# Optimization experiments

Measured on AMD Instinct MI355X. Metric: run time of the kernel, lower is better.

Reference implementation:

```python
import jax, jax.numpy as jnp
import numpy as np

N_NODES = 50000
N_EDGES = 800000
D = 128
N_LAYERS = 3
BN_EPS = 1e-5


def setup_inputs() -> dict:
    key = jax.random.key(0)
    ks = jax.random.split(key, 12)
    x = jax.random.normal(ks[0], (N_NODES, D), dtype=jnp.float32)
    edge_index = jax.random.randint(ks[1], (2, N_EDGES), 0, N_NODES, dtype=jnp.int64)
    edge_attr = jnp.zeros((N_EDGES,), dtype=jnp.int32)  # unused by BaseGIN
    edge_weight = jax.random.uniform(ks[2], (N_EDGES,), dtype=jnp.float32)
    s = 1.0 / np.sqrt(D)
    W1 = jax.random.uniform(ks[3], (N_LAYERS, D, D), minval=-s, maxval=s, dtype=jnp.float32)
    b1 = jax.random.uniform(ks[4], (N_LAYERS, D), minval=-s, maxval=s, dtype=jnp.float32)
    W2 = jax.random.uniform(ks[5], (N_LAYERS, D, D), minval=-s, maxval=s, dtype=jnp.float32)
    b2 = jax.random.uniform(ks[6], (N_LAYERS, D), minval=-s, maxval=s, dtype=jnp.float32)
    eps = jnp.zeros((N_LAYERS,), dtype=jnp.float32)          # GIN epsilon, init 0
    gamma = jnp.ones((N_LAYERS, D), dtype=jnp.float32)       # BN weight
    beta = jnp.zeros((N_LAYERS, D), dtype=jnp.float32)       # BN bias
    return {"x": x, "edge_index": edge_index, "edge_attr": edge_attr,
            "edge_weight": edge_weight, "W1": W1, "b1": b1, "W2": W2,
            "b2": b2, "eps": eps, "gamma": gamma, "beta": beta}


def reference(x, edge_index, edge_attr, edge_weight, W1, b1, W2, b2, eps, gamma, beta):
    del edge_attr  # deleted in BaseGIN.forward
    src, dst = edge_index[0], edge_index[1]
    ew = edge_weight[:, None]  # [E, 1], matches edge_weight[:, None] in torch
    n = x.shape[0]
    for i in range(N_LAYERS):
        # GINConv: propagate = scatter-add of gathered x[src] * edge_weight
        msg = x[src] * ew                                   # [E, D]
        agg = jax.ops.segment_sum(msg, dst, num_segments=n)  # [N, D]
        h = (1.0 + eps[i]) * x + agg
        # MLP: Linear -> ReLU -> Linear
        h = jnp.maximum(h @ W1[i] + b1[i], 0.0) @ W2[i] + b2[i]
        # BatchNorm1d (training-mode batch statistics, biased variance)
        mu = jnp.mean(h, axis=0)
        var = jnp.mean((h - mu) ** 2, axis=0)
        h = gamma[i] * (h - mu) * jax.lax.rsqrt(var + BN_EPS) + beta[i]
        h = jnp.maximum(h, 0.0)  # ReLU (dropout p=0.0 -> identity)
        x = x + h  # residual
    return x
```

## Files before the change

kernel.cpp:

```cpp
#include <hip/hip_runtime.h>

#define NN 50000
#define NE 800000
#define DD 128
#define D4 32
#define NBUCK 196
#define CAP 5120
#define BIN_EDGES 2048

typedef __attribute__((ext_vector_type(8))) short short8;
typedef __attribute__((ext_vector_type(4))) float f32x4;

__device__ __forceinline__ unsigned short f2bf(float f) {
    unsigned u = __float_as_uint(f);
    unsigned r = u + 0x7FFF + ((u >> 16) & 1);
    return (unsigned short)(r >> 16);
}
__device__ __forceinline__ float bf2f(unsigned short s) {
    return __uint_as_float(((unsigned)s) << 16);
}


__global__ void x2b(const float4* __restrict__ xin, ushort4* __restrict__ xb) {
    int i = blockIdx.x * blockDim.x + threadIdx.x;
    if (i >= NN * D4) return;
    float4 v = xin[i];
    ushort4 o;
    o.x = f2bf(v.x); o.y = f2bf(v.y); o.z = f2bf(v.z); o.w = f2bf(v.w);
    xb[i] = o;
}


__global__ void prep_wt(const float* __restrict__ W1, const float* __restrict__ W2,
                        unsigned short* __restrict__ Wt) {
    int i = blockIdx.x * blockDim.x + threadIdx.x;
    if (i >= 6 * 16384) return;
    int m = i >> 14;
    int r = i & 16383;
    int n = r >> 7;
    int k = r & 127;
    const float* Ws = (m < 3) ? (W1 + m * 16384) : (W2 + (m - 3) * 16384);
    Wt[i] = f2bf(Ws[k * 128 + n]);
}


__global__ void init_bcur(int* __restrict__ bcur) {
    int t = threadIdx.x;
    if (t < NBUCK) bcur[t] = t * CAP;
}

__global__ void __launch_bounds__(256) bin_pass(const int* __restrict__ ei,
                                                const float* __restrict__ ew,
                                                int* __restrict__ bcur,
                                                int2* __restrict__ staging) {
    __shared__ int cnt[256], base[256], cur[256];
    int tid = threadIdx.x;
    int e0 = blockIdx.x * BIN_EDGES;
    int ne = NE - e0; if (ne > BIN_EDGES) ne = BIN_EDGES;
    cnt[tid] = 0;
    cur[tid] = 0;
    __syncthreads();
    int dstv[BIN_EDGES / 256];
    unsigned packv[BIN_EDGES / 256];
#pragma unroll
    for (int j = 0; j < BIN_EDGES / 256; j++) {
        int i = j * 256 + tid;
        dstv[j] = -1;
        if (i < ne) {
            int e = e0 + i;
            int dst = ei[NE + e];
            dstv[j] = dst;
            packv[j] = (((unsigned)ei[e]) << 16) | (unsigned)f2bf(ew[e]);
            atomicAdd(&cnt[dst >> 8], 1);
        }
    }
    __syncthreads();
    if (tid < NBUCK && cnt[tid] > 0) base[tid] = atomicAdd(&bcur[tid], cnt[tid]);
    __syncthreads();
#pragma unroll
    for (int j = 0; j < BIN_EDGES / 256; j++) {
        int dst = dstv[j];
        if (dst >= 0) {
            int b = dst >> 8;
            int p = atomicAdd(&cur[b], 1);
            staging[base[b] + p] = make_int2((int)packv[j], dst & 255);
        }
    }
}

__global__ void scan_buckets(const int* __restrict__ bcur, int* __restrict__ bb2) {
    __shared__ int sh[256];
    int tid = threadIdx.x;
    int c = (tid < NBUCK) ? (bcur[tid] - tid * CAP) : 0;
    sh[tid] = c;
    __syncthreads();
    for (int o = 1; o < 256; o <<= 1) {
        int v = sh[tid];
        int add = (tid >= o) ? sh[tid - o] : 0;
        __syncthreads();
        sh[tid] = v + add;
        __syncthreads();
    }
    if (tid < NBUCK) bb2[tid] = sh[tid] - c;
}

__global__ void __launch_bounds__(256) place_pass(const int2* __restrict__ staging,
                                                  const int* __restrict__ bcur,
                                                  const int* __restrict__ bb2,
                                                  int* __restrict__ rowptr,
                                                  unsigned* __restrict__ srcw) {
    __shared__ int hist[256], off[256], cur[256];
    __shared__ unsigned outb[CAP];
    int b = blockIdx.x;
    int tid = threadIdx.x;
    int sbase = b * CAP;
    int nb = bcur[b] - sbase;
    int bucketBase = bb2[b];
    hist[tid] = 0;
    __syncthreads();
    for (int i = tid; i < nb; i += 256) atomicAdd(&hist[staging[sbase + i].y], 1);
    __syncthreads();
    off[tid] = hist[tid];
    __syncthreads();
    for (int o = 1; o < 256; o <<= 1) {
        int v = off[tid];
        int add = (tid >= o) ? off[tid - o] : 0;
        __syncthreads();
        off[tid] = v + add;
        __syncthreads();
    }
    int excl = off[tid] - hist[tid];
    cur[tid] = excl;
    int node = b * 256 + tid;
    if (node < NN) rowptr[node] = bucketBase + excl;
    if (b == 0 && tid == 0) rowptr[NN] = NE;
    __syncthreads();
    for (int i = tid; i < nb; i += 256) {
        int2 r = staging[sbase + i];
        int p = atomicAdd(&cur[r.y], 1);
        outb[p] = (unsigned)r.x;
    }
    __syncthreads();
    for (int i = tid; i < nb; i += 256) srcw[bucketBase + i] = outb[i];
}


__global__ void __launch_bounds__(256) gather_kernel(
    const unsigned short* __restrict__ xb, const unsigned* __restrict__ srcw,
    const int* __restrict__ rowptr, const float* __restrict__ epsp,
    unsigned short* __restrict__ g, float* __restrict__ stats) {
    if (blockIdx.x == 0) stats[threadIdx.x] = 0.f;
    int node = blockIdx.x * 8 + (threadIdx.x >> 5);
    int lane = threadIdx.x & 31;
    if (node >= NN) return;
    float epsv = 1.0f + *epsp;
    int beg = rowptr[node], end = rowptr[node + 1];
    const ushort4* xb4 = (const ushort4*)xb;
    ushort4 xv = xb4[node * D4 + lane];
    float4 acc = make_float4(bf2f(xv.x) * epsv, bf2f(xv.y) * epsv,
                             bf2f(xv.z) * epsv, bf2f(xv.w) * epsv);
    int i = beg;
    for (; i + 1 < end; i += 2) {
        unsigned sw0 = srcw[i];
        unsigned sw1 = srcw[i + 1];
        ushort4 r0 = xb4[(sw0 >> 16) * D4 + lane];
        ushort4 r1 = xb4[(sw1 >> 16) * D4 + lane];
        float w0 = bf2f((unsigned short)(sw0 & 0xffff));
        float w1 = bf2f((unsigned short)(sw1 & 0xffff));
        acc.x += bf2f(r0.x) * w0; acc.y += bf2f(r0.y) * w0;
        acc.z += bf2f(r0.z) * w0; acc.w += bf2f(r0.w) * w0;
        acc.x += bf2f(r1.x) * w1; acc.y += bf2f(r1.y) * w1;
        acc.z += bf2f(r1.z) * w1; acc.w += bf2f(r1.w) * w1;
    }
    if (i < end) {
        unsigned sw = srcw[i];
        ushort4 r = xb4[(sw >> 16) * D4 + lane];
        float w = bf2f((unsigned short)(sw & 0xffff));
        acc.x += bf2f(r.x) * w; acc.y += bf2f(r.y) * w;
        acc.z += bf2f(r.z) * w; acc.w += bf2f(r.w) * w;
    }
    ushort4 o;
    o.x = f2bf(acc.x); o.y = f2bf(acc.y); o.z = f2bf(acc.z); o.w = f2bf(acc.w);
    ((ushort4*)g)[node * D4 + lane] = o;
}


#define GM 64

template <int MODE>
__global__ void __launch_bounds__(256) mfma_gemm(
    const unsigned short* __restrict__ A,
    const unsigned short* __restrict__ Wt,
    const float* __restrict__ bias,
    unsigned short* __restrict__ outB, float* __restrict__ stats) {
    __shared__ unsigned short As[GM * 128];

    int tid = threadIdx.x;
    int wave = tid >> 6;
    int lane = tid & 63;
    int q = lane >> 4;
    int ml = lane & 15;
    int r0 = blockIdx.x * GM;

#pragma unroll
    for (int i = 0; i < GM / 16; i++) {
        int idx = i * 256 + tid;
        int row = idx >> 4;
        int c = idx & 15;
        float4 v = make_float4(0.f, 0.f, 0.f, 0.f);
        int grow = r0 + row;
        if (grow < NN) v = *(const float4*)(A + grow * DD + c * 8);
        int cs = c ^ (row & 15);
        *(float4*)(&As[row * DD + cs * 8]) = v;
    }

    short8 Bf[2][4];
#pragma unroll
    for (int t = 0; t < 2; t++)
#pragma unroll
        for (int ks = 0; ks < 4; ks++) {
            int n = wave * 32 + t * 16 + ml;
            Bf[t][ks] = *(const short8*)(Wt + n * DD + ks * 32 + q * 8);
        }

    float bvl[2] = {bias[wave * 32 + ml], bias[wave * 32 + 16 + ml]};

    __syncthreads();

    float s[2] = {0.f, 0.f}, s2[2] = {0.f, 0.f};

    for (int rt = 0; rt < GM / 16; rt++) {
        int arow = rt * 16 + ml;
        short8 Af[4];
#pragma unroll
        for (int ks = 0; ks < 4; ks++) {
            int cs = (ks * 4 + q) ^ (arow & 15);
            Af[ks] = *(const short8*)(&As[arow * DD + cs * 8]);
        }
        f32x4 acc[2] = {{0.f, 0.f, 0.f, 0.f}, {0.f, 0.f, 0.f, 0.f}};
#pragma unroll
        for (int ks = 0; ks < 4; ks++) {
            acc[0] = __builtin_amdgcn_mfma_f32_16x16x32_bf16(Af[ks], Bf[0][ks], acc[0], 0, 0, 0);
            acc[1] = __builtin_amdgcn_mfma_f32_16x16x32_bf16(Af[ks], Bf[1][ks], acc[1], 0, 0, 0);
        }
#pragma unroll
        for (int t = 0; t < 2; t++) {
            int col = wave * 32 + t * 16 + ml;
#pragma unroll
            for (int r = 0; r < 4; r++) {
                int grow = r0 + rt * 16 + q * 4 + r;
                if (grow < NN) {
                    float v = acc[t][r] + bvl[t];
                    if (MODE == 0) {
                        outB[grow * DD + col] = f2bf(fmaxf(v, 0.f));
                    } else {
                        outB[grow * DD + col] = f2bf(v);
                        s[t] += v;
                        s2[t] += v * v;
                    }
                }
            }
        }
    }

    if (MODE == 1) {
#pragma unroll
        for (int t = 0; t < 2; t++) {
            float a = s[t], b = s2[t];
            a += __shfl_xor(a, 16); b += __shfl_xor(b, 16);
            a += __shfl_xor(a, 32); b += __shfl_xor(b, 32);
            if (q == 0) {
                int col = wave * 32 + t * 16 + ml;
                atomicAdd(&stats[col], a);
                atomicAdd(&stats[DD + col], b);
            }
        }
    }
}


__global__ void bn_apply(const unsigned short* __restrict__ hb, const float* __restrict__ stats,
                         const float* __restrict__ gamma, const float* __restrict__ beta,
                         const unsigned short* __restrict__ xbin, ushort4* __restrict__ xbout,
                         float4* __restrict__ xf32) {
    int i = blockIdx.x * blockDim.x + threadIdx.x;
    if (i >= NN * D4) return;
    int c4 = i & 31;
    const float invN = 1.0f / NN;
    float4 s = ((const float4*)stats)[c4];
    float4 s2 = ((const float4*)stats)[D4 + c4];
    float4 mu = make_float4(s.x * invN, s.y * invN, s.z * invN, s.w * invN);
    float4 var = make_float4(s2.x * invN - mu.x * mu.x, s2.y * invN - mu.y * mu.y,
                             s2.z * invN - mu.z * mu.z, s2.w * invN - mu.w * mu.w);
    float4 inv = make_float4(rsqrtf(var.x + 1e-5f), rsqrtf(var.y + 1e-5f),
                             rsqrtf(var.z + 1e-5f), rsqrtf(var.w + 1e-5f));
    float4 g = ((const float4*)gamma)[c4];
    float4 b = ((const float4*)beta)[c4];
    ushort4 hu = ((const ushort4*)hb)[i];
    float4 hv = make_float4(bf2f(hu.x), bf2f(hu.y), bf2f(hu.z), bf2f(hu.w));
    ushort4 xu = ((const ushort4*)xbin)[i];
    float4 xv = make_float4(bf2f(xu.x), bf2f(xu.y), bf2f(xu.z), bf2f(xu.w));
    float4 v = make_float4(fmaxf(g.x * (hv.x - mu.x) * inv.x + b.x, 0.f),
                           fmaxf(g.y * (hv.y - mu.y) * inv.y + b.y, 0.f),
                           fmaxf(g.z * (hv.z - mu.z) * inv.z + b.z, 0.f),
                           fmaxf(g.w * (hv.w - mu.w) * inv.w + b.w, 0.f));
    float4 o = make_float4(xv.x + v.x, xv.y + v.y, xv.z + v.z, xv.w + v.w);
    if (xbout) {
        ushort4 ob;
        ob.x = f2bf(o.x); ob.y = f2bf(o.y); ob.z = f2bf(o.z); ob.w = f2bf(o.w);
        xbout[i] = ob;
    }
    if (xf32) xf32[i] = o;
}


extern "C" void kernel_launch(void* const* d_in, const int* in_sizes, int n_in,
                              void* d_out, int out_size, void* d_ws, size_t ws_size,
                              hipStream_t stream) {
    const float* x_in = (const float*)d_in[0];
    const int* ei = (const int*)d_in[1];
    const float* ew = (const float*)d_in[3];
    const float* W1 = (const float*)d_in[4];
    const float* b1 = (const float*)d_in[5];
    const float* W2 = (const float*)d_in[6];
    const float* b2 = (const float*)d_in[7];
    const float* eps = (const float*)d_in[8];
    const float* gamma = (const float*)d_in[9];
    const float* beta = (const float*)d_in[10];

    float* x = (float*)d_out;

    char* ws = (char*)d_ws;
    unsigned short* g = (unsigned short*)ws;
    unsigned short* t = (unsigned short*)(ws + 12800000);
    unsigned short* hb = (unsigned short*)(ws + 25600000);
    int2* staging = (int2*)(ws + 25600000);
    unsigned short* xb = (unsigned short*)(ws + 38400000);
    float* stats = (float*)(ws + 51200000);
    int* rowptr = (int*)(ws + 51201024);
    unsigned short* Wtall = (unsigned short*)(ws + 51401216);
    unsigned* srcw = (unsigned*)(ws + 51597824);
    int* bcur = (int*)(ws + 54797824);
    int* bb2 = (int*)(ws + 54798848);

    const int n4x = NN * D4;

    init_bcur<<<1, 256, 0, stream>>>(bcur);
    bin_pass<<<(NE + BIN_EDGES - 1) / BIN_EDGES, 256, 0, stream>>>(ei, ew, bcur, staging);
    scan_buckets<<<1, 256, 0, stream>>>(bcur, bb2);
    place_pass<<<NBUCK, 256, 0, stream>>>(staging, bcur, bb2, rowptr, srcw);

    prep_wt<<<(6 * 16384 + 255) / 256, 256, 0, stream>>>(W1, W2, Wtall);

    x2b<<<(n4x + 255) / 256, 256, 0, stream>>>((const float4*)x_in, (ushort4*)xb);

    const int gemmGrid = (NN + GM - 1) / GM;

    for (int i = 0; i < 3; i++) {
        const float* b1i = b1 + i * DD;
        const float* b2i = b2 + i * DD;
        const unsigned short* Wt1 = Wtall + i * 16384;
        const unsigned short* Wt2 = Wtall + (3 + i) * 16384;

        gather_kernel<<<(NN + 7) / 8, 256, 0, stream>>>(xb, srcw, rowptr, eps + i, g, stats);

        mfma_gemm<0><<<gemmGrid, 256, 0, stream>>>(g, Wt1, b1i, t, nullptr);

        mfma_gemm<1><<<gemmGrid, 256, 0, stream>>>(t, Wt2, b2i, hb, stats);

        bn_apply<<<(n4x + 255) / 256, 256, 0, stream>>>(
            hb, stats, gamma + i * DD, beta + i * DD, xb,
            (i < 2) ? (ushort4*)xb : nullptr,
            (i == 2) ? (float4*)x : nullptr);
    }
}
```

Baseline: 387.9 us.

## Fuse two MLP GEMMs via shared-memory intermediate, merge setup kernels, unroll gather

The two per-layer MFMA GEMMs are merged into one kernel that keeps the ReLU'd hidden tile in swizzled LDS instead of writing it to global memory and reading it back. This removes a 12.8MB round trip and one launch per layer, at the cost of doubling LDS and the registers that hold weight fragments. The three setup kernels (x to bf16, weight transpose, bucket init) become one launch, and the gather loop is unrolled to four edges so more loads are in flight. The workspace layout is compacted because the intermediate buffer is gone.

Result: faster. 347.4 us (-10.4%).

```diff
diff --git a/kernel.cpp b/kernel.cpp
--- a/kernel.cpp
+++ b/kernel.cpp
@@ -21,33 +21,33 @@
 }
 
 
-__global__ void x2b(const float4* __restrict__ xin, ushort4* __restrict__ xb) {
-    int i = blockIdx.x * blockDim.x + threadIdx.x;
-    if (i >= NN * D4) return;
-    float4 v = xin[i];
-    ushort4 o;
-    o.x = f2bf(v.x); o.y = f2bf(v.y); o.z = f2bf(v.z); o.w = f2bf(v.w);
-    xb[i] = o;
-}
-
-
-__global__ void prep_wt(const float* __restrict__ W1, const float* __restrict__ W2,
-                        unsigned short* __restrict__ Wt) {
-    int i = blockIdx.x * blockDim.x + threadIdx.x;
-    if (i >= 6 * 16384) return;
-    int m = i >> 14;
-    int r = i & 16383;
-    int n = r >> 7;
-    int k = r & 127;
-    const float* Ws = (m < 3) ? (W1 + m * 16384) : (W2 + (m - 3) * 16384);
-    Wt[i] = f2bf(Ws[k * 128 + n]);
-}
-
-
-__global__ void init_bcur(int* __restrict__ bcur) {
-    int t = threadIdx.x;
-    if (t < NBUCK) bcur[t] = t * CAP;
-}
+#define X2B_NB 6250
+#define WT_NB 384
+
+__global__ void setup_kernel(const float4* __restrict__ xin, const float* __restrict__ W1,
+                             const float* __restrict__ W2, ushort4* __restrict__ xb,
+                             unsigned short* __restrict__ Wt, int* __restrict__ bcur) {
+    int bid = blockIdx.x;
+    int tid = threadIdx.x;
+    if (bid < X2B_NB) {
+        int i = bid * 256 + tid;
+        float4 v = xin[i];
+        ushort4 o;
+        o.x = f2bf(v.x); o.y = f2bf(v.y); o.z = f2bf(v.z); o.w = f2bf(v.w);
+        xb[i] = o;
+    } else if (bid < X2B_NB + WT_NB) {
+        int i = (bid - X2B_NB) * 256 + tid;
+        int m = i >> 14;
+        int r = i & 16383;
+        int n = r >> 7;
+        int k = r & 127;
+        const float* Ws = (m < 3) ? (W1 + m * 16384) : (W2 + (m - 3) * 16384);
+        Wt[i] = f2bf(Ws[k * 128 + n]);
+    } else {
+        if (tid < NBUCK) bcur[tid] = tid * CAP;
+    }
+}
+
 
 __global__ void __launch_bounds__(256) bin_pass(const int* __restrict__ ei,
                                                 const float* __restrict__ ew,
@@ -160,19 +160,26 @@
     float4 acc = make_float4(bf2f(xv.x) * epsv, bf2f(xv.y) * epsv,
                              bf2f(xv.z) * epsv, bf2f(xv.w) * epsv);
     int i = beg;
-    for (; i + 1 < end; i += 2) {
-        unsigned sw0 = srcw[i];
-        unsigned sw1 = srcw[i + 1];
+    for (; i + 3 < end; i += 4) {
+        unsigned sw0 = srcw[i], sw1 = srcw[i + 1], sw2 = srcw[i + 2], sw3 = srcw[i + 3];
         ushort4 r0 = xb4[(sw0 >> 16) * D4 + lane];
         ushort4 r1 = xb4[(sw1 >> 16) * D4 + lane];
+        ushort4 r2 = xb4[(sw2 >> 16) * D4 + lane];
+        ushort4 r3 = xb4[(sw3 >> 16) * D4 + lane];
         float w0 = bf2f((unsigned short)(sw0 & 0xffff));
         float w1 = bf2f((unsigned short)(sw1 & 0xffff));
+        float w2 = bf2f((unsigned short)(sw2 & 0xffff));
+        float w3 = bf2f((unsigned short)(sw3 & 0xffff));
         acc.x += bf2f(r0.x) * w0; acc.y += bf2f(r0.y) * w0;
         acc.z += bf2f(r0.z) * w0; acc.w += bf2f(r0.w) * w0;
         acc.x += bf2f(r1.x) * w1; acc.y += bf2f(r1.y) * w1;
         acc.z += bf2f(r1.z) * w1; acc.w += bf2f(r1.w) * w1;
-    }
-    if (i < end) {
+        acc.x += bf2f(r2.x) * w2; acc.y += bf2f(r2.y) * w2;
+        acc.z += bf2f(r2.z) * w2; acc.w += bf2f(r2.w) * w2;
+        acc.x += bf2f(r3.x) * w3; acc.y += bf2f(r3.y) * w3;
+        acc.z += bf2f(r3.z) * w3; acc.w += bf2f(r3.w) * w3;
+    }
+    for (; i < end; i++) {
         unsigned sw = srcw[i];
         ushort4 r = xb4[(sw >> 16) * D4 + lane];
         float w = bf2f((unsigned short)(sw & 0xffff));
@@ -187,13 +194,14 @@
 
 #define GM 64
 
-template <int MODE>
-__global__ void __launch_bounds__(256) mfma_gemm(
+__global__ void __launch_bounds__(256) mlp_fused(
     const unsigned short* __restrict__ A,
-    const unsigned short* __restrict__ Wt,
-    const float* __restrict__ bias,
+    const unsigned short* __restrict__ Wt1,
+    const unsigned short* __restrict__ Wt2,
+    const float* __restrict__ b1, const float* __restrict__ b2,
     unsigned short* __restrict__ outB, float* __restrict__ stats) {
     __shared__ unsigned short As[GM * 128];
+    __shared__ unsigned short Ts[GM * 128];
 
     int tid = threadIdx.x;
     int wave = tid >> 6;
@@ -214,20 +222,19 @@
         *(float4*)(&As[row * DD + cs * 8]) = v;
     }
 
-    short8 Bf[2][4];
+    short8 Bf1[2][4], Bf2[2][4];
 #pragma unroll
     for (int t = 0; t < 2; t++)
 #pragma unroll
         for (int ks = 0; ks < 4; ks++) {
             int n = wave * 32 + t * 16 + ml;
-            Bf[t][ks] = *(const short8*)(Wt + n * DD + ks * 32 + q * 8);
-        }
-
-    float bvl[2] = {bias[wave * 32 + ml], bias[wave * 32 + 16 + ml]};
-
-    __syncthreads();
-
-    float s[2] = {0.f, 0.f}, s2[2] = {0.f, 0.f};
+            Bf1[t][ks] = *(const short8*)(Wt1 + n * DD + ks * 32 + q * 8);
+            Bf2[t][ks] = *(const short8*)(Wt2 + n * DD + ks * 32 + q * 8);
+        }
+    float bvl1[2] = {b1[wave * 32 + ml], b1[wave * 32 + 16 + ml]};
+    float bvl2[2] = {b2[wave * 32 + ml], b2[wave * 32 + 16 + ml]};
+
+    __syncthreads();
 
     for (int rt = 0; rt < GM / 16; rt++) {
         int arow = rt * 16 + ml;
@@ -240,8 +247,36 @@
         f32x4 acc[2] = {{0.f, 0.f, 0.f, 0.f}, {0.f, 0.f, 0.f, 0.f}};
 #pragma unroll
         for (int ks = 0; ks < 4; ks++) {
-            acc[0] = __builtin_amdgcn_mfma_f32_16x16x32_bf16(Af[ks], Bf[0][ks], acc[0], 0, 0, 0);
-            acc[1] = __builtin_amdgcn_mfma_f32_16x16x32_bf16(Af[ks], Bf[1][ks], acc[1], 0, 0, 0);
+            acc[0] = __builtin_amdgcn_mfma_f32_16x16x32_bf16(Af[ks], Bf1[0][ks], acc[0], 0, 0, 0);
+            acc[1] = __builtin_amdgcn_mfma_f32_16x16x32_bf16(Af[ks], Bf1[1][ks], acc[1], 0, 0, 0);
+        }
+#pragma unroll
+        for (int t = 0; t < 2; t++) {
+            int col = wave * 32 + t * 16 + ml;
+#pragma unroll
+            for (int r = 0; r < 4; r++) {
+                int lrow = rt * 16 + q * 4 + r;
+                unsigned short u = f2bf(fmaxf(acc[t][r] + bvl1[t], 0.f));
+                Ts[lrow * DD + ((((col >> 3) ^ (lrow & 15)) << 3) | (col & 7))] = u;
+            }
+        }
+    }
+    __syncthreads();
+
+    float s[2] = {0.f, 0.f}, s2[2] = {0.f, 0.f};
+    for (int rt = 0; rt < GM / 16; rt++) {
+        int arow = rt * 16 + ml;
+        short8 Af[4];
+#pragma unroll
+        for (int ks = 0; ks < 4; ks++) {
+            int cs = (ks * 4 + q) ^ (arow & 15);
+            Af[ks] = *(const short8*)(&Ts[arow * DD + cs * 8]);
+        }
+        f32x4 acc[2] = {{0.f, 0.f, 0.f, 0.f}, {0.f, 0.f, 0.f, 0.f}};
+#pragma unroll
+        for (int ks = 0; ks < 4; ks++) {
+            acc[0] = __builtin_amdgcn_mfma_f32_16x16x32_bf16(Af[ks], Bf2[0][ks], acc[0], 0, 0, 0);
+            acc[1] = __builtin_amdgcn_mfma_f32_16x16x32_bf16(Af[ks], Bf2[1][ks], acc[1], 0, 0, 0);
         }
 #pragma unroll
         for (int t = 0; t < 2; t++) {
@@ -250,30 +285,24 @@
             for (int r = 0; r < 4; r++) {
                 int grow = r0 + rt * 16 + q * 4 + r;
                 if (grow < NN) {
-                    float v = acc[t][r] + bvl[t];
-                    if (MODE == 0) {
-                        outB[grow * DD + col] = f2bf(fmaxf(v, 0.f));
-                    } else {
-                        outB[grow * DD + col] = f2bf(v);
-                        s[t] += v;
-                        s2[t] += v * v;
-                    }
+                    float v = acc[t][r] + bvl2[t];
+                    outB[grow * DD + col] = f2bf(v);
+                    s[t] += v;
+                    s2[t] += v * v;
                 }
             }
         }
     }
 
-    if (MODE == 1) {
-#pragma unroll
-        for (int t = 0; t < 2; t++) {
-            float a = s[t], b = s2[t];
-            a += __shfl_xor(a, 16); b += __shfl_xor(b, 16);
-            a += __shfl_xor(a, 32); b += __shfl_xor(b, 32);
-            if (q == 0) {
-                int col = wave * 32 + t * 16 + ml;
-                atomicAdd(&stats[col], a);
-                atomicAdd(&stats[DD + col], b);
-            }
+#pragma unroll
+    for (int t = 0; t < 2; t++) {
+        float a = s[t], b = s2[t];
+        a += __shfl_xor(a, 16); b += __shfl_xor(b, 16);
+        a += __shfl_xor(a, 32); b += __shfl_xor(b, 32);
+        if (q == 0) {
+            int col = wave * 32 + t * 16 + ml;
+            atomicAdd(&stats[col], a);
+            atomicAdd(&stats[DD + col], b);
         }
     }
 }
@@ -332,41 +361,34 @@
 
     char* ws = (char*)d_ws;
     unsigned short* g = (unsigned short*)ws;
-    unsigned short* t = (unsigned short*)(ws + 12800000);
-    unsigned short* hb = (unsigned short*)(ws + 25600000);
-    int2* staging = (int2*)(ws + 25600000);
-    unsigned short* xb = (unsigned short*)(ws + 38400000);
-    float* stats = (float*)(ws + 51200000);
-    int* rowptr = (int*)(ws + 51201024);
-    unsigned short* Wtall = (unsigned short*)(ws + 51401216);
-    unsigned* srcw = (unsigned*)(ws + 51597824);
-    int* bcur = (int*)(ws + 54797824);
-    int* bb2 = (int*)(ws + 54798848);
+    unsigned short* hb = (unsigned short*)(ws + 12800000);
+    int2* staging = (int2*)(ws + 12800000);
+    unsigned short* xb = (unsigned short*)(ws + 25600000);
+    float* stats = (float*)(ws + 38400000);
+    int* rowptr = (int*)(ws + 38401024);
+    unsigned short* Wtall = (unsigned short*)(ws + 38601216);
+    unsigned* srcw = (unsigned*)(ws + 38797824);
+    int* bcur = (int*)(ws + 41997824);
+    int* bb2 = (int*)(ws + 41998848);
 
     const int n4x = NN * D4;
 
-    init_bcur<<<1, 256, 0, stream>>>(bcur);
+    setup_kernel<<<X2B_NB + WT_NB + 1, 256, 0, stream>>>(
+        (const float4*)x_in, W1, W2, (ushort4*)xb, Wtall, bcur);
+
     bin_pass<<<(NE + BIN_EDGES - 1) / BIN_EDGES, 256, 0, stream>>>(ei, ew, bcur, staging);
     scan_buckets<<<1, 256, 0, stream>>>(bcur, bb2);
     place_pass<<<NBUCK, 256, 0, stream>>>(staging, bcur, bb2, rowptr, srcw);
 
-    prep_wt<<<(6 * 16384 + 255) / 256, 256, 0, stream>>>(W1, W2, Wtall);
-
-    x2b<<<(n4x + 255) / 256, 256, 0, stream>>>((const float4*)x_in, (ushort4*)xb);
-
     const int gemmGrid = (NN + GM - 1) / GM;
 
     for (int i = 0; i < 3; i++) {
-        const float* b1i = b1 + i * DD;
-        const float* b2i = b2 + i * DD;
         const unsigned short* Wt1 = Wtall + i * 16384;
         const unsigned short* Wt2 = Wtall + (3 + i) * 16384;
 
         gather_kernel<<<(NN + 7) / 8, 256, 0, stream>>>(xb, srcw, rowptr, eps + i, g, stats);
 
-        mfma_gemm<0><<<gemmGrid, 256, 0, stream>>>(g, Wt1, b1i, t, nullptr);
-
-        mfma_gemm<1><<<gemmGrid, 256, 0, stream>>>(t, Wt2, b2i, hb, stats);
+        mlp_fused<<<gemmGrid, 256, 0, stream>>>(g, Wt1, Wt2, b1 + i * DD, b2 + i * DD, hb, stats);
 
         bn_apply<<<(n4x + 255) / 256, 256, 0, stream>>>(
             hb, stats, gamma + i * DD, beta + i * DD, xb,
```
